# Optimization experiments

Measured on AMD Instinct MI355X. Metric: run time of the kernel, lower is better.

The kernel has to match this reference:

```python
import jax, jax.numpy as jnp
import numpy as np

EMBED_DIM = 1024
NUM_HEADS = 16
HEAD_DIM = EMBED_DIM // NUM_HEADS
B, S = 2, 2048
NEG = -1e20


def setup_inputs() -> dict:
    key = jax.random.key(0)
    ks = jax.random.split(key, 8)
    scale = 0.02
    return {
        "query": jax.random.normal(ks[0], (B, S, EMBED_DIM), jnp.float32),
        "keys": jax.random.normal(ks[1], (B, S, EMBED_DIM), jnp.float32),
        "values": jax.random.normal(ks[2], (B, S, EMBED_DIM), jnp.float32),
        "mask": jax.random.randint(ks[3], (1, 1, S, S), 0, 2, jnp.int32),
        "Wq": jax.random.normal(ks[4], (EMBED_DIM, EMBED_DIM), jnp.float32) * scale,
        "Wk": jax.random.normal(ks[5], (EMBED_DIM, EMBED_DIM), jnp.float32) * scale,
        "Wv": jax.random.normal(ks[6], (EMBED_DIM, EMBED_DIM), jnp.float32) * scale,
        "Wo": jax.random.normal(ks[7], (EMBED_DIM, EMBED_DIM), jnp.float32) * scale,
        "bo": jnp.zeros((EMBED_DIM,), jnp.float32),
    }


def reference(query, keys, values, mask, Wq, Wk, Wv, Wo, bo):
    N, Lq, _ = query.shape
    Lk = keys.shape[1]
    # torch nn.Linear: y = x @ W.T  (bias=False for Q/K/V)
    Q = (query @ Wq.T).reshape(N, Lq, NUM_HEADS, HEAD_DIM)
    K = (keys @ Wk.T).reshape(N, Lk, NUM_HEADS, HEAD_DIM)
    V = (values @ Wv.T).reshape(N, Lk, NUM_HEADS, HEAD_DIM)
    # NOTE: source scales by sqrt(embed_dim), not sqrt(head_dim) — kept faithful.
    energy = jnp.einsum("nqhd,nkhd->nhqk", Q, K) / jnp.sqrt(
        jnp.asarray(EMBED_DIM, Q.dtype)
    )
    energy = jnp.where(mask == 0, jnp.asarray(NEG, energy.dtype), energy)
    attention = jax.nn.softmax(energy, axis=3)
    out = jnp.einsum("nhqk,nkhd->nqhd", attention, V).reshape(N, Lq, EMBED_DIM)
    return out @ Wo.T + bo
```

## Files before the change

### kernel.cpp

```cpp
#include <hip/hip_runtime.h>
#include <stdint.h>

typedef __bf16 bf16;
typedef __bf16 bf16x4 __attribute__((ext_vector_type(4)));
typedef __bf16 bf16x8 __attribute__((ext_vector_type(8)));
typedef float f32x4 __attribute__((ext_vector_type(4)));
typedef float f32x16 __attribute__((ext_vector_type(16)));
typedef unsigned int uintx2 __attribute__((ext_vector_type(2)));
typedef unsigned int uintx4 __attribute__((ext_vector_type(4)));

#define MFMA16(a, b, c) __builtin_amdgcn_mfma_f32_16x16x32_bf16((a), (b), (c), 0, 0, 0)
#define MFMA32(a, b, c) __builtin_amdgcn_mfma_f32_32x32x16_bf16((a), (b), (c), 0, 0, 0)

__device__ __forceinline__ void gload16(const bf16* g, bf16* l) {
    __builtin_amdgcn_global_load_lds(
        (const __attribute__((address_space(1))) void*)g,
        (__attribute__((address_space(3))) void*)l, 16, 0, 0);
}

__device__ __forceinline__ float fast_exp2(float x) {
#if __has_builtin(__builtin_amdgcn_exp2f)
    return __builtin_amdgcn_exp2f(x);
#else
    return exp2f(x);
#endif
}

__global__ __launch_bounds__(256) void cvt_kernel(
    const float* __restrict__ q, const float* __restrict__ k, const float* __restrict__ v,
    const float* __restrict__ wq, const float* __restrict__ wk,
    const float* __restrict__ wv, const float* __restrict__ wo,
    bf16* __restrict__ qb, bf16* __restrict__ kb, bf16* __restrict__ vb,
    bf16* __restrict__ wqb, bf16* __restrict__ wkb, bf16* __restrict__ wvb,
    bf16* __restrict__ wob)
{
    int z = blockIdx.z;
    const float* src; bf16* dst; int n;
    switch (z) {
        case 0:  src = q;  dst = qb;  n = 4194304; break;
        case 1:  src = k;  dst = kb;  n = 4194304; break;
        case 2:  src = v;  dst = vb;  n = 4194304; break;
        case 3:  src = wq; dst = wqb; n = 1048576; break;
        case 4:  src = wk; dst = wkb; n = 1048576; break;
        case 5:  src = wv; dst = wvb; n = 1048576; break;
        default: src = wo; dst = wob; n = 1048576; break;
    }
    int i = (blockIdx.x * 256 + threadIdx.x) * 8;
    if (i >= n) return;
    float4 f0 = *(const float4*)(src + i);
    float4 f1 = *(const float4*)(src + i + 4);
    bf16x8 o;
    o[0] = (bf16)f0.x; o[1] = (bf16)f0.y; o[2] = (bf16)f0.z; o[3] = (bf16)f0.w;
    o[4] = (bf16)f1.x; o[5] = (bf16)f1.y; o[6] = (bf16)f1.z; o[7] = (bf16)f1.w;
    *(bf16x8*)(dst + i) = o;
}

__global__ __launch_bounds__(256) void maskpack_kernel(
    const int* __restrict__ mask, unsigned long long* __restrict__ maskb)
{
    int gid  = blockIdx.x * 256 + threadIdx.x;
    int word = gid >> 6;
    int lane = gid & 63;
    int row = word >> 5, wc = word & 31;
    int mv = mask[row * 2048 + wc * 64 + lane];
    unsigned long long bits = __ballot(mv != 0);
    if (lane == 0) maskb[word] = bits;
}

template <int OUTMODE, int MT>
__global__ __launch_bounds__(256) void gemm_kernel(
    const bf16* __restrict__ A0, const bf16* __restrict__ A1, const bf16* __restrict__ A2,
    const bf16* __restrict__ B0, const bf16* __restrict__ B1, const bf16* __restrict__ B2,
    bf16* __restrict__ C0, bf16* __restrict__ C1, bf16* __restrict__ C2,
    const float* __restrict__ bias, float* __restrict__ outf)
{
    constexpr int MI = (MT == 128) ? 4 : 2;

    const int z = blockIdx.z;
    const bf16* A = (z == 0) ? A0 : (z == 1) ? A1 : A2;
    const bf16* B = (z == 0) ? B0 : (z == 1) ? B1 : B2;

    __shared__ bf16 At[MT * 32];
    __shared__ bf16 Bt[128 * 32];

    const int tid  = threadIdx.x;
    const int lane = tid & 63;
    const int wave = tid >> 6;
    const int quad = lane >> 4;
    const int l16  = lane & 15;
    const int wm = (wave >> 1) * (MT / 2);
    const int wn = (wave & 1) * 64;
    const int m0 = blockIdx.y * MT;
    const int n0 = blockIdx.x * 128;

    const int lrow = lane >> 2;
    const int lcol = (lane & 3) * 8;

    f32x4 acc[MI][4] = {};

    const bf16* Ag = A + (size_t)(m0 + lrow) * 1024 + lcol;
    const bf16* Bg = B + (size_t)(n0 + lrow) * 1024 + lcol;

    for (int k0 = 0; k0 < 1024; k0 += 32) {
        __syncthreads();
        if constexpr (MT == 128) {
#pragma unroll
            for (int j = 0; j < 2; ++j)
                gload16(Ag + (size_t)(wave * 32 + j * 16) * 1024 + k0,
                        At + (wave * 32 + j * 16) * 32);
        } else {
            gload16(Ag + (size_t)(wave * 16) * 1024 + k0, At + (wave * 16) * 32);
        }
#pragma unroll
        for (int j = 0; j < 2; ++j)
            gload16(Bg + (size_t)(wave * 32 + j * 16) * 1024 + k0,
                    Bt + (wave * 32 + j * 16) * 32);
        __syncthreads();

        bf16x8 af[MI], bg[4];
#pragma unroll
        for (int i = 0; i < MI; ++i)
            af[i] = *(const bf16x8*)(At + (wm + i * 16 + l16) * 32 + quad * 8);
#pragma unroll
        for (int j = 0; j < 4; ++j)
            bg[j] = *(const bf16x8*)(Bt + (wn + j * 16 + l16) * 32 + quad * 8);
#pragma unroll
        for (int i = 0; i < MI; ++i)
#pragma unroll
            for (int j = 0; j < 4; ++j)
                acc[i][j] = MFMA16(af[i], bg[j], acc[i][j]);
    }

    if constexpr (OUTMODE == 0) {
        bf16* C = (z == 0) ? C0 : (z == 1) ? C1 : C2;
        const float cs = (z == 0) ? 0.0450842200277800f : 1.0f;
#pragma unroll
        for (int i = 0; i < MI; ++i)
#pragma unroll
            for (int j = 0; j < 4; ++j) {
                int row = m0 + wm + i * 16 + quad * 4;
                int col = n0 + wn + j * 16 + l16;
#pragma unroll
                for (int r = 0; r < 4; ++r)
                    C[(row + r) * 1024 + col] = (bf16)(acc[i][j][r] * cs);
            }
    } else {
#pragma unroll
        for (int j = 0; j < 4; ++j) {
            int col = n0 + wn + j * 16 + l16;
            float bj = bias[col];
#pragma unroll
            for (int i = 0; i < MI; ++i) {
                int row = m0 + wm + i * 16 + quad * 4;
#pragma unroll
                for (int r = 0; r < 4; ++r)
                    outf[(row + r) * 1024 + col] = acc[i][j][r] + bj;
            }
        }
    }
}

__global__ __launch_bounds__(256) void transpose_kernel(const bf16* __restrict__ V,
                                                        bf16* __restrict__ Vt)
{
    __shared__ bf16 t[64][72];
    const int tid = threadIdx.x;
    const int b  = blockIdx.z;
    const int s0 = blockIdx.x * 64;
    const int d0 = blockIdx.y * 64;
#pragma unroll
    for (int c = 0; c < 2; ++c) {
        int qq = c * 256 + tid;
        int row = qq >> 3, col = (qq & 7) * 8;
        *(uint4*)(&t[row][col]) =
            *(const uint4*)(V + (size_t)(b * 2048 + s0 + row) * 1024 + d0 + col);
    }
    __syncthreads();
#pragma unroll
    for (int c = 0; c < 2; ++c) {
        int qq = c * 256 + tid;
        int drow = qq >> 3, scol = (qq & 7) * 8;
        bf16x8 o;
#pragma unroll
        for (int j = 0; j < 8; ++j) {
            int sidx  = scol + j;
            int sperm = (sidx & ~12) | ((sidx & 4) << 1) | ((sidx & 8) >> 1);
            o[j] = t[sperm][drow];
        }
        *(bf16x8*)(Vt + (size_t)(b * 1024 + d0 + drow) * 2048 + s0 + scol) = o;
    }
}

__global__ __launch_bounds__(512, 4) void flash_kernel(
    const bf16* __restrict__ Q, const bf16* __restrict__ K, const bf16* __restrict__ Vt,
    const unsigned long long* __restrict__ maskb, bf16* __restrict__ O)
{
    __shared__ char smem[65536];

    const int tid  = threadIdx.x;
    const int lane = tid & 63;
    const int wave = tid >> 6;
    const int half = wave >> 2;
    const int w4   = wave & 3;
    const int l32  = lane & 31;
    const int hl   = lane >> 5;
    const int l7   = lane & 7;
    const int b  = blockIdx.z;
    const int h  = blockIdx.y;
    const int q0 = blockIdx.x * 128;
    const int qt = q0 + w4 * 32;

    bf16* hbase = (bf16*)smem + half * 16384;
    bf16* K0 = hbase;
    bf16* K1 = hbase + 4096;
    bf16* V0 = hbase + 8192;
    bf16* V1 = hbase + 12288;

    const bf16* Qb = Q + (size_t)(b * 2048 + qt + l32) * 1024 + h * 64 + hl * 8;
    bf16x8 qf[4];
#pragma unroll
    for (int ks = 0; ks < 4; ++ks) qf[ks] = *(const bf16x8*)(Qb + ks * 16);

    bf16x8 ones;
#pragma unroll
    for (int j = 0; j < 8; ++j) ones[j] = (bf16)1.0f;

    f32x16 acc[2] = {};
    f32x16 lacc = {};

    const int dmarow = lane >> 3;
    const int dmacol = (l7 ^ dmarow) * 8;
    const bf16* Kg = K + (size_t)(b * 2048 + w4 * 16 + dmarow) * 1024 + h * 64 + dmacol;
    const bf16* Vg = Vt + (size_t)((b * 16 + h) * 64 + w4 * 16 + dmarow) * 2048 + dmacol;
    const unsigned long long* Mg = maskb + (size_t)(qt + l32) * 32 + half * 16;
    const int kbase = half * 1024;

    auto stage = [&](bf16* Kd, bf16* Vd, int ktAbs) {
        gload16(Kg + (size_t)ktAbs * 1024,       Kd + (w4 * 16) * 64);
        gload16(Kg + (size_t)(ktAbs + 8) * 1024, Kd + (w4 * 16 + 8) * 64);
        gload16(Vg + ktAbs,                      Vd + (w4 * 16) * 64);
        gload16(Vg + ktAbs + 8 * 2048,           Vd + (w4 * 16 + 8) * 64);
    };

    unsigned long long mw = Mg[0];
    stage(K0, V0, kbase);

    auto body = [&](const bf16* Kc, const bf16* Vc, bf16* Kn, bf16* Vn, int it) {
        __syncthreads();
        unsigned long long mw_next = 0;
        if (it + 1 < 16) {
            stage(Kn, Vn, kbase + (it + 1) * 64);
            mw_next = Mg[it + 1];
        }

        bf16x8 pa[4];
#pragma unroll
        for (int t = 0; t < 2; ++t) {
            f32x16 s = {};
#pragma unroll
            for (int ks = 0; ks < 4; ++ks) {
                bf16x8 ka = *(const bf16x8*)(Kc + (t * 32 + l32) * 64 +
                                             (((ks * 2 + hl) ^ l7) * 8));
                s = MFMA32(ka, qf[ks], s);
            }
            unsigned mwt = (unsigned)(mw >> (t * 32 + 4 * hl));
            unsigned W[4][2];
#pragma unroll
            for (int g = 0; g < 4; ++g) {
                bf16x4 pv;
#pragma unroll
                for (int r = 0; r < 4; ++r) {
                    float ev = fast_exp2(s[g * 4 + r]);
                    pv[r] = (mwt & (1u << (8 * g + r))) ? (bf16)ev : (bf16)0.0f;
                }
                uintx2 u = __builtin_bit_cast(uintx2, pv);
                W[g][0] = u[0];
                W[g][1] = u[1];
            }
#pragma unroll
            for (int kh = 0; kh < 2; ++kh) {
                uintx4 aw = { W[2 * kh][0], W[2 * kh][1],
                              W[2 * kh + 1][0], W[2 * kh + 1][1] };
                pa[t * 2 + kh] = __builtin_bit_cast(bf16x8, aw);
            }
        }

#pragma unroll
        for (int dt = 0; dt < 2; ++dt)
#pragma unroll
            for (int ks = 0; ks < 4; ++ks) {
                bf16x8 vb = *(const bf16x8*)(Vc + (dt * 32 + l32) * 64 +
                                             (((ks * 2 + hl) ^ l7) * 8));
                acc[dt] = MFMA32(pa[ks], vb, acc[dt]);
            }
#pragma unroll
        for (int ks = 0; ks < 4; ++ks)
            lacc = MFMA32(pa[ks], ones, lacc);

        mw = mw_next;
    };

    for (int it = 0; it < 16; it += 2) {
        body(K0, V0, K1, V1, it);
        body(K1, V1, K0, V0, it + 1);
    }

    __syncthreads();
    float* cb = (float*)smem;
    float* ex = cb + (w4 * 64 + lane) * 4;
    if (half == 1) {
#pragma unroll
        for (int i = 0; i < 4; ++i) {
            f32x4 t0, t1, t2;
#pragma unroll
            for (int j = 0; j < 4; ++j) {
                t0[j] = acc[0][i * 4 + j];
                t1[j] = acc[1][i * 4 + j];
                t2[j] = lacc[i * 4 + j];
            }
            *(f32x4*)(ex + (i + 0) * 1024) = t0;
            *(f32x4*)(ex + (i + 4) * 1024) = t1;
            *(f32x4*)(ex + (i + 8) * 1024) = t2;
        }
    }
    __syncthreads();
    if (half == 0) {
#pragma unroll
        for (int i = 0; i < 4; ++i) {
            f32x4 t0 = *(const f32x4*)(ex + (i + 0) * 1024);
            f32x4 t1 = *(const f32x4*)(ex + (i + 4) * 1024);
            f32x4 t2 = *(const f32x4*)(ex + (i + 8) * 1024);
#pragma unroll
            for (int j = 0; j < 4; ++j) {
                acc[0][i * 4 + j] += t0[j];
                acc[1][i * 4 + j] += t1[j];
                lacc[i * 4 + j]   += t2[j];
            }
        }

        const size_t obase = (size_t)(b * 2048 + qt) * 1024 + h * 64;
#pragma unroll
        for (int g = 0; g < 4; ++g)
#pragma unroll
            for (int r = 0; r < 4; ++r) {
                int qr = 4 * hl + 8 * g + r;
                float inv = 1.0f / lacc[g * 4 + r];
                O[obase + (size_t)qr * 1024 + l32]      = (bf16)(acc[0][g * 4 + r] * inv);
                O[obase + (size_t)qr * 1024 + 32 + l32] = (bf16)(acc[1][g * 4 + r] * inv);
            }
    }
}

extern "C" void kernel_launch(void* const* d_in, const int* in_sizes, int n_in,
                              void* d_out, int out_size, void* d_ws, size_t ws_size,
                              hipStream_t stream)
{
    const float* q  = (const float*)d_in[0];
    const float* k  = (const float*)d_in[1];
    const float* v  = (const float*)d_in[2];
    const int* mask = (const int*)d_in[3];
    const float* wq = (const float*)d_in[4];
    const float* wk = (const float*)d_in[5];
    const float* wv = (const float*)d_in[6];
    const float* wo = (const float*)d_in[7];
    const float* bo = (const float*)d_in[8];
    float* out = (float*)d_out;

    char* p = (char*)d_ws;
    auto alloc = [&](size_t bytes) {
        char* r = p;
        p += (bytes + 255) & ~(size_t)255;
        return r;
    };
    const size_t SB = (size_t)4096 * 1024 * 2;
    const size_t WB = (size_t)1024 * 1024 * 2;
    bf16* qb  = (bf16*)alloc(SB);
    bf16* kb  = (bf16*)alloc(SB);
    bf16* vb  = (bf16*)alloc(SB);
    bf16* wqb = (bf16*)alloc(WB);
    bf16* wkb = (bf16*)alloc(WB);
    bf16* wvb = (bf16*)alloc(WB);
    bf16* wob = (bf16*)alloc(WB);
    bf16* Qp  = (bf16*)alloc(SB);
    bf16* Kp  = (bf16*)alloc(SB);
    bf16* Vp  = (bf16*)alloc(SB);
    bf16* Vtp = (bf16*)alloc(SB);
    bf16* Ob  = (bf16*)alloc(SB);
    unsigned long long* maskb = (unsigned long long*)alloc(2048 * 32 * 8);

    cvt_kernel<<<dim3(2048, 1, 7), 256, 0, stream>>>(
        q, k, v, wq, wk, wv, wo, qb, kb, vb, wqb, wkb, wvb, wob);

    maskpack_kernel<<<dim3(16384), 256, 0, stream>>>(mask, maskb);

    gemm_kernel<0, 128><<<dim3(8, 32, 3), 256, 0, stream>>>(
        qb, kb, vb, wqb, wkb, wvb, Qp, Kp, Vp, nullptr, nullptr);

    transpose_kernel<<<dim3(32, 16, 2), 256, 0, stream>>>(Vp, Vtp);

    flash_kernel<<<dim3(16, 16, 2), 512, 0, stream>>>(Qp, Kp, Vtp, maskb, Ob);

    gemm_kernel<1, 64><<<dim3(8, 64, 1), 256, 0, stream>>>(
        Ob, nullptr, nullptr, wob, nullptr, nullptr,
        nullptr, nullptr, nullptr, bo, out);
}
```

Before: 240.6 us.

## Fuse mask packing into convert, V transpose into GEMM; remap flash blocks, add setprio

Mask bit-packing moves into the convert kernel as an extra z-slice, and the V transpose moves into the QKV GEMM epilogue through a padded shared-memory tile, which removes two kernel launches and the Vp round trip. The flash kernel remaps block indices so each XCD handles whole (batch, head) groups, aiming at better L2 reuse of K/V. It also raises wave priority around the MFMA sections. The GEMM epilogue now needs a larger shared buffer and an extra sync, which could lower occupancy for that kernel.

```diff
diff --git a/kernel.cpp b/kernel.cpp
--- a/kernel.cpp
+++ b/kernel.cpp
@@ -30,11 +30,23 @@
     const float* __restrict__ q, const float* __restrict__ k, const float* __restrict__ v,
     const float* __restrict__ wq, const float* __restrict__ wk,
     const float* __restrict__ wv, const float* __restrict__ wo,
+    const int* __restrict__ mask,
     bf16* __restrict__ qb, bf16* __restrict__ kb, bf16* __restrict__ vb,
     bf16* __restrict__ wqb, bf16* __restrict__ wkb, bf16* __restrict__ wvb,
-    bf16* __restrict__ wob)
+    bf16* __restrict__ wob, unsigned long long* __restrict__ maskb)
 {
     int z = blockIdx.z;
+    if (z == 7) {
+#pragma unroll
+        for (int it = 0; it < 8; ++it) {
+            int gid  = it * 524288 + blockIdx.x * 256 + threadIdx.x;
+            int lane = gid & 63;
+            int mv = mask[gid];
+            unsigned long long bits = __ballot(mv != 0);
+            if (lane == 0) maskb[gid >> 6] = bits;
+        }
+        return;
+    }
     const float* src; bf16* dst; int n;
     switch (z) {
         case 0:  src = q;  dst = qb;  n = 4194304; break;
@@ -55,33 +67,22 @@
     *(bf16x8*)(dst + i) = o;
 }
 
-__global__ __launch_bounds__(256) void maskpack_kernel(
-    const int* __restrict__ mask, unsigned long long* __restrict__ maskb)
-{
-    int gid  = blockIdx.x * 256 + threadIdx.x;
-    int word = gid >> 6;
-    int lane = gid & 63;
-    int row = word >> 5, wc = word & 31;
-    int mv = mask[row * 2048 + wc * 64 + lane];
-    unsigned long long bits = __ballot(mv != 0);
-    if (lane == 0) maskb[word] = bits;
-}
-
 template <int OUTMODE, int MT>
 __global__ __launch_bounds__(256) void gemm_kernel(
     const bf16* __restrict__ A0, const bf16* __restrict__ A1, const bf16* __restrict__ A2,
     const bf16* __restrict__ B0, const bf16* __restrict__ B1, const bf16* __restrict__ B2,
-    bf16* __restrict__ C0, bf16* __restrict__ C1, bf16* __restrict__ C2,
+    bf16* __restrict__ C0, bf16* __restrict__ C1, bf16* __restrict__ Vt,
     const float* __restrict__ bias, float* __restrict__ outf)
 {
     constexpr int MI = (MT == 128) ? 4 : 2;
+    constexpr int SMEM = (OUTMODE == 0 && MT == 128) ? (128 * 136) : (MT * 32 + 128 * 32);
+    __shared__ bf16 smem[SMEM];
+    bf16* At = smem;
+    bf16* Bt = smem + MT * 32;
 
     const int z = blockIdx.z;
     const bf16* A = (z == 0) ? A0 : (z == 1) ? A1 : A2;
     const bf16* B = (z == 0) ? B0 : (z == 1) ? B1 : B2;
-
-    __shared__ bf16 At[MT * 32];
-    __shared__ bf16 Bt[128 * 32];
 
     const int tid  = threadIdx.x;
     const int lane = tid & 63;
@@ -132,7 +133,36 @@
     }
 
     if constexpr (OUTMODE == 0) {
-        bf16* C = (z == 0) ? C0 : (z == 1) ? C1 : C2;
+        if (MT == 128 && z == 2) {
+            __syncthreads();
+            const int qsw = ((quad & 1) << 1) | (quad >> 1);
+#pragma unroll
+            for (int i = 0; i < MI; ++i)
+#pragma unroll
+                for (int j = 0; j < 4; ++j) {
+                    int e  = wn + j * 16 + l16;
+                    int sp = wm + i * 16 + qsw * 4;
+                    bf16x4 v4;
+#pragma unroll
+                    for (int r = 0; r < 4; ++r) v4[r] = (bf16)acc[i][j][r];
+                    *(bf16x4*)(smem + e * 136 + sp) = v4;
+                }
+            __syncthreads();
+            const int bq = m0 >> 11;
+            const int srow = m0 & 2047;
+#pragma unroll
+            for (int c = 0; c < 2; ++c) {
+                int idx = c * 256 + tid;
+                int e = idx >> 2, sc = (idx & 3) * 32;
+                bf16* dst = Vt + (size_t)(bq * 1024 + n0 + e) * 2048 + srow + sc;
+#pragma unroll
+                for (int kk = 0; kk < 4; ++kk)
+                    *(bf16x8*)(dst + kk * 8) =
+                        *(const bf16x8*)(smem + e * 136 + sc + kk * 8);
+            }
+            return;
+        }
+        bf16* C = (z == 0) ? C0 : C1;
         const float cs = (z == 0) ? 0.0450842200277800f : 1.0f;
 #pragma unroll
         for (int i = 0; i < MI; ++i)
@@ -157,37 +187,6 @@
                     outf[(row + r) * 1024 + col] = acc[i][j][r] + bj;
             }
         }
-    }
-}
-
-__global__ __launch_bounds__(256) void transpose_kernel(const bf16* __restrict__ V,
-                                                        bf16* __restrict__ Vt)
-{
-    __shared__ bf16 t[64][72];
-    const int tid = threadIdx.x;
-    const int b  = blockIdx.z;
-    const int s0 = blockIdx.x * 64;
-    const int d0 = blockIdx.y * 64;
-#pragma unroll
-    for (int c = 0; c < 2; ++c) {
-        int qq = c * 256 + tid;
-        int row = qq >> 3, col = (qq & 7) * 8;
-        *(uint4*)(&t[row][col]) =
-            *(const uint4*)(V + (size_t)(b * 2048 + s0 + row) * 1024 + d0 + col);
-    }
-    __syncthreads();
-#pragma unroll
-    for (int c = 0; c < 2; ++c) {
-        int qq = c * 256 + tid;
-        int drow = qq >> 3, scol = (qq & 7) * 8;
-        bf16x8 o;
-#pragma unroll
-        for (int j = 0; j < 8; ++j) {
-            int sidx  = scol + j;
-            int sperm = (sidx & ~12) | ((sidx & 4) << 1) | ((sidx & 8) >> 1);
-            o[j] = t[sperm][drow];
-        }
-        *(bf16x8*)(Vt + (size_t)(b * 1024 + d0 + drow) * 2048 + s0 + scol) = o;
     }
 }
 
@@ -205,9 +204,14 @@
     const int l32  = lane & 31;
     const int hl   = lane >> 5;
     const int l7   = lane & 7;
-    const int b  = blockIdx.z;
-    const int h  = blockIdx.y;
-    const int q0 = blockIdx.x * 128;
+
+    const int flat = blockIdx.x + 16 * (blockIdx.y + 16 * blockIdx.z);
+    const int xcd  = flat & 7;
+    const int slot = flat >> 3;
+    const int bh   = xcd * 4 + (slot >> 4);
+    const int h  = bh & 15;
+    const int b  = bh >> 4;
+    const int q0 = (slot & 15) * 128;
     const int qt = q0 + w4 * 32;
 
     bf16* hbase = (bf16*)smem + half * 16384;
@@ -257,12 +261,14 @@
 #pragma unroll
         for (int t = 0; t < 2; ++t) {
             f32x16 s = {};
+            __builtin_amdgcn_s_setprio(1);
 #pragma unroll
             for (int ks = 0; ks < 4; ++ks) {
                 bf16x8 ka = *(const bf16x8*)(Kc + (t * 32 + l32) * 64 +
                                              (((ks * 2 + hl) ^ l7) * 8));
                 s = MFMA32(ka, qf[ks], s);
             }
+            __builtin_amdgcn_s_setprio(0);
             unsigned mwt = (unsigned)(mw >> (t * 32 + 4 * hl));
             unsigned W[4][2];
 #pragma unroll
@@ -285,6 +291,7 @@
             }
         }
 
+        __builtin_amdgcn_s_setprio(1);
 #pragma unroll
         for (int dt = 0; dt < 2; ++dt)
 #pragma unroll
@@ -296,6 +303,7 @@
 #pragma unroll
         for (int ks = 0; ks < 4; ++ks)
             lacc = MFMA32(pa[ks], ones, lacc);
+        __builtin_amdgcn_s_setprio(0);
 
         mw = mw_next;
     };
@@ -383,20 +391,15 @@
     bf16* wob = (bf16*)alloc(WB);
     bf16* Qp  = (bf16*)alloc(SB);
     bf16* Kp  = (bf16*)alloc(SB);
-    bf16* Vp  = (bf16*)alloc(SB);
     bf16* Vtp = (bf16*)alloc(SB);
     bf16* Ob  = (bf16*)alloc(SB);
     unsigned long long* maskb = (unsigned long long*)alloc(2048 * 32 * 8);
 
-    cvt_kernel<<<dim3(2048, 1, 7), 256, 0, stream>>>(
-        q, k, v, wq, wk, wv, wo, qb, kb, vb, wqb, wkb, wvb, wob);
-
-    maskpack_kernel<<<dim3(16384), 256, 0, stream>>>(mask, maskb);
+    cvt_kernel<<<dim3(2048, 1, 8), 256, 0, stream>>>(
+        q, k, v, wq, wk, wv, wo, mask, qb, kb, vb, wqb, wkb, wvb, wob, maskb);
 
     gemm_kernel<0, 128><<<dim3(8, 32, 3), 256, 0, stream>>>(
-        qb, kb, vb, wqb, wkb, wvb, Qp, Kp, Vp, nullptr, nullptr);
-
-    transpose_kernel<<<dim3(32, 16, 2), 256, 0, stream>>>(Vp, Vtp);
+        qb, kb, vb, wqb, wkb, wvb, Qp, Kp, Vtp, nullptr, nullptr);
 
     flash_kernel<<<dim3(16, 16, 2), 512, 0, stream>>>(Qp, Kp, Vtp, maskb, Ob);
 
```

Result: faster. 233.0 us (-3.2%).
